# Kernel tuning notes

Hardware: AMD Instinct MI355X
Metric: run time of the kernel (lower is better)

Reference implementation:

```python
import jax, jax.numpy as jnp
import numpy as np

D = 1024
S = 4096

def setup_inputs() -> dict:
    key = jax.random.key(0)
    ks = jax.random.split(key, 7)
    x = jax.random.normal(ks[0], (S, D), dtype=jnp.float32)
    scale = 1.0 / np.sqrt(D)
    wq = jax.random.normal(ks[1], (D, D), dtype=jnp.float32) * scale
    wk = jax.random.normal(ks[2], (D, D), dtype=jnp.float32) * scale
    wv = jax.random.normal(ks[3], (D, D), dtype=jnp.float32) * scale
    bq = jax.random.normal(ks[4], (D,), dtype=jnp.float32) * 0.01
    bk = jax.random.normal(ks[5], (D,), dtype=jnp.float32) * 0.01
    bv = jax.random.normal(ks[6], (D,), dtype=jnp.float32) * 0.01
    return {"x": x, "wq": wq, "bq": bq, "wk": wk, "bk": bk, "wv": wv, "bv": bv}

def reference(x, wq, bq, wk, bk, wv, bv):
    # q = x @ wq^T + bq  (torch nn.Linear convention: weight [out,in])
    q = x @ wq.T + bq            # [S, D]
    k = x @ wk.T + bk            # [S, D]
    v = x @ wv.T + bv            # [S, D]
    inv_sqrt_d = 1.0 / jnp.sqrt(jnp.asarray(x.shape[1], dtype=x.dtype))
    scores = (q @ k.T) * inv_sqrt_d      # [S, S]
    attn = jax.nn.softmax(scores, axis=-1)
    return attn @ v                      # [S, D]
```

## Files before the change

### kernel.cpp

```cpp
#include <hip/hip_runtime.h>
#include <stdint.h>
#include <stddef.h>

#define SEQ 4096
#define DIM 1024

typedef __bf16 bf16x8 __attribute__((ext_vector_type(8)));
typedef float floatx4 __attribute__((ext_vector_type(4)));
typedef unsigned short u16x8 __attribute__((ext_vector_type(8)));

__device__ __forceinline__ unsigned short f2b(float f) {
  union { float f; unsigned u; } v; v.f = f;
  unsigned u = v.u;
  unsigned r = (u + 0x7FFFu + ((u >> 16) & 1u)) >> 16;
  return (unsigned short)r;
}
__device__ __forceinline__ float b2f(unsigned short h) {
  union { unsigned u; float f; } v; v.u = ((unsigned)h) << 16;
  return v.f;
}

__global__ __launch_bounds__(256)
void cvt_all(const float* __restrict__ x, const float* __restrict__ wq,
             const float* __restrict__ wk, const float* __restrict__ wv,
             unsigned short* __restrict__ xb, unsigned short* __restrict__ wqb,
             unsigned short* __restrict__ wkb, unsigned short* __restrict__ wvb) {
  const int bid = blockIdx.x;
  const float* src;
  unsigned short* dst;
  int off;
  if (bid < 4096)      { src = x;  dst = xb;  off = bid; }
  else if (bid < 5120) { src = wq; dst = wqb; off = bid - 4096; }
  else if (bid < 6144) { src = wk; dst = wkb; off = bid - 5120; }
  else                 { src = wv; dst = wvb; off = bid - 6144; }
  const int i = off * 1024 + threadIdx.x * 4;
  float4 f = *(const float4*)(src + i);
  ushort4 o;
  o.x = f2b(f.x); o.y = f2b(f.y); o.z = f2b(f.z); o.w = f2b(f.w);
  *(ushort4*)(dst + i) = o;
}

__device__ __forceinline__ void swizzle_tiles(int gx, int gy, int& bx, int& by) {
  const int pid = blockIdx.y * gx + blockIdx.x;
  const int GM = 8;
  const int group = pid / (GM * gx);
  const int first = group * GM;
  const int gsz = (gy - first) < GM ? (gy - first) : GM;
  by = first + (pid % gsz);
  bx = (pid % (GM * gx)) / gsz;
}

__device__ __forceinline__ void gemm_core128(
    const unsigned short* __restrict__ A,
    const unsigned short* __restrict__ B,
    int lda, int ldb, int kext,
    unsigned short* As, unsigned short* Bs,
    floatx4 acc[4][4]) {
  const int tid  = threadIdx.x;
  const int lane = tid & 63;
  const int wave = tid >> 6;
  const int sub_m = (wave >> 1) * 64;
  const int sub_n = (wave & 1) * 64;
  const int col  = lane & 15;
  const int quad = lane >> 4;

  const int srow  = tid >> 3;
  const int sgran = (tid & 7) ^ (srow & 7);
  const int scol  = sgran * 8;
  const int dflat = tid * 8;

  const unsigned short* Ag = A + (size_t)srow * lda + scol;
  const unsigned short* Bg = B + (size_t)srow * ldb + scol;

  for (int k0 = 0; k0 < kext; k0 += 64) {
    __syncthreads();
#pragma unroll
    for (int j = 0; j < 4; j++) {
      __builtin_amdgcn_global_load_lds(
          (const __attribute__((address_space(1))) void*)(Ag + (size_t)(j * 32) * lda + k0),
          (__attribute__((address_space(3))) void*)(&As[j * 2048 + dflat]), 16, 0, 0);
      __builtin_amdgcn_global_load_lds(
          (const __attribute__((address_space(1))) void*)(Bg + (size_t)(j * 32) * ldb + k0),
          (__attribute__((address_space(3))) void*)(&Bs[j * 2048 + dflat]), 16, 0, 0);
    }
    __syncthreads();
#pragma unroll
    for (int ks = 0; ks < 64; ks += 32) {
      const int gbase = ks >> 3;
      bf16x8 af[4], bfr[4];
#pragma unroll
      for (int i = 0; i < 4; i++) {
        const int R = sub_m + 16 * i + col;
        const int slot = (gbase + quad) ^ (R & 7);
        af[i] = *(const bf16x8*)&As[R * 64 + slot * 8];
      }
#pragma unroll
      for (int j = 0; j < 4; j++) {
        const int R = sub_n + 16 * j + col;
        const int slot = (gbase + quad) ^ (R & 7);
        bfr[j] = *(const bf16x8*)&Bs[R * 64 + slot * 8];
      }
#pragma unroll
      for (int i = 0; i < 4; i++)
#pragma unroll
        for (int j = 0; j < 4; j++)
          acc[i][j] = __builtin_amdgcn_mfma_f32_16x16x32_bf16(af[i], bfr[j],
                                                              acc[i][j], 0, 0, 0);
    }
  }
}

__device__ __forceinline__ void gemm_core64(
    const unsigned short* __restrict__ A,
    const unsigned short* __restrict__ B,
    int lda, int ldb, int kext,
    unsigned short* As, unsigned short* Bs,
    floatx4 acc[4][2]) {
  const int tid  = threadIdx.x;
  const int lane = tid & 63;
  const int wave = tid >> 6;
  const int sub_n = wave * 32;
  const int col  = lane & 15;
  const int quad = lane >> 4;

  const int srow  = tid >> 3;
  const int sgran = (tid & 7) ^ (srow & 7);
  const int scol  = sgran * 8;
  const int dflat = tid * 8;

  const unsigned short* Ag = A + (size_t)srow * lda + scol;
  const unsigned short* Bg = B + (size_t)srow * ldb + scol;

  for (int k0 = 0; k0 < kext; k0 += 64) {
    __syncthreads();
#pragma unroll
    for (int j = 0; j < 2; j++)
      __builtin_amdgcn_global_load_lds(
          (const __attribute__((address_space(1))) void*)(Ag + (size_t)(j * 32) * lda + k0),
          (__attribute__((address_space(3))) void*)(&As[j * 2048 + dflat]), 16, 0, 0);
#pragma unroll
    for (int j = 0; j < 4; j++)
      __builtin_amdgcn_global_load_lds(
          (const __attribute__((address_space(1))) void*)(Bg + (size_t)(j * 32) * ldb + k0),
          (__attribute__((address_space(3))) void*)(&Bs[j * 2048 + dflat]), 16, 0, 0);
    __syncthreads();
#pragma unroll
    for (int ks = 0; ks < 64; ks += 32) {
      const int gbase = ks >> 3;
      bf16x8 af[4], bfr[2];
#pragma unroll
      for (int i = 0; i < 4; i++) {
        const int R = 16 * i + col;
        const int slot = (gbase + quad) ^ (R & 7);
        af[i] = *(const bf16x8*)&As[R * 64 + slot * 8];
      }
#pragma unroll
      for (int j = 0; j < 2; j++) {
        const int R = sub_n + 16 * j + col;
        const int slot = (gbase + quad) ^ (R & 7);
        bfr[j] = *(const bf16x8*)&Bs[R * 64 + slot * 8];
      }
#pragma unroll
      for (int i = 0; i < 4; i++)
#pragma unroll
        for (int j = 0; j < 2; j++)
          acc[i][j] = __builtin_amdgcn_mfma_f32_16x16x32_bf16(af[i], bfr[j],
                                                              acc[i][j], 0, 0, 0);
    }
  }
}


__global__ __launch_bounds__(256, 2)
void qkv_gemm(const unsigned short* __restrict__ xb,
              const unsigned short* __restrict__ wqb,
              const unsigned short* __restrict__ wkb,
              const unsigned short* __restrict__ wvb,
              const float* __restrict__ bq, const float* __restrict__ bk,
              const float* __restrict__ bv,
              unsigned short* __restrict__ qb, unsigned short* __restrict__ kb,
              unsigned short* __restrict__ vtb) {
  __shared__ unsigned short As[8192];
  __shared__ unsigned short Bs[8192];
  const int z = blockIdx.z;
  const int pid = blockIdx.x;

  floatx4 acc[4][4];
#pragma unroll
  for (int i = 0; i < 4; i++)
#pragma unroll
    for (int j = 0; j < 4; j++) acc[i][j] = (floatx4)0.0f;

  const int lane = threadIdx.x & 63;
  const int wave = threadIdx.x >> 6;
  const int sub_m = (wave >> 1) * 64;
  const int sub_n = (wave & 1) * 64;
  const int col  = lane & 15;
  const int quad = lane >> 4;

  if (z < 2) {
    const unsigned short* W = z ? wkb : wqb;
    const float* bias = z ? bk : bq;
    unsigned short* outp = z ? kb : qb;
    const int by = pid >> 3, bx = pid & 7;
    const int tile_m = by * 128, tile_n = bx * 128;

    gemm_core128(xb + (size_t)tile_m * DIM, W + (size_t)tile_n * DIM,
                 DIM, DIM, DIM, As, Bs, acc);

    float biasv[4];
#pragma unroll
    for (int j = 0; j < 4; j++) biasv[j] = bias[tile_n + sub_n + 16 * j + col];
#pragma unroll
    for (int i = 0; i < 4; i++)
#pragma unroll
      for (int j = 0; j < 4; j++)
#pragma unroll
        for (int r = 0; r < 4; r++) {
          const int m = tile_m + sub_m + 16 * i + quad * 4 + r;
          const int n = tile_n + sub_n + 16 * j + col;
          outp[(size_t)m * DIM + n] = f2b(acc[i][j][r] + biasv[j]);
        }
  } else {
    const int by = pid >> 5, bx = pid & 31;
    const int tile_m = by * 128, tile_n = bx * 128;

    gemm_core128(wvb + (size_t)tile_m * DIM, xb + (size_t)tile_n * DIM,
                 DIM, DIM, DIM, As, Bs, acc);

#pragma unroll
    for (int i = 0; i < 4; i++) {
      const float* bp = &bv[tile_m + sub_m + 16 * i + quad * 4];
      float bm[4];
#pragma unroll
      for (int r = 0; r < 4; r++) bm[r] = bp[r];
#pragma unroll
      for (int j = 0; j < 4; j++)
#pragma unroll
        for (int r = 0; r < 4; r++) {
          const int m = tile_m + sub_m + 16 * i + quad * 4 + r;
          const int n = tile_n + sub_n + 16 * j + col;
          vtb[(size_t)m * SEQ + n] = f2b(acc[i][j][r] + bm[r]);
        }
    }
  }
}

__global__ __launch_bounds__(256, 2)
void score_gemm(const unsigned short* __restrict__ qb,
                const unsigned short* __restrict__ kb,
                unsigned short* __restrict__ sc, float scale) {
  __shared__ unsigned short As[8192];
  __shared__ unsigned short Bs[8192];
  int bx, by;
  swizzle_tiles(gridDim.x, gridDim.y, bx, by);
  const int tile_m = by * 128;
  const int tile_n = bx * 128;

  floatx4 acc[4][4];
#pragma unroll
  for (int i = 0; i < 4; i++)
#pragma unroll
    for (int j = 0; j < 4; j++) acc[i][j] = (floatx4)0.0f;

  gemm_core128(qb + (size_t)tile_m * DIM, kb + (size_t)tile_n * DIM,
               DIM, DIM, DIM, As, Bs, acc);

  const int lane = threadIdx.x & 63;
  const int wave = threadIdx.x >> 6;
  const int sub_m = (wave >> 1) * 64;
  const int sub_n = (wave & 1) * 64;
  const int col  = lane & 15;
  const int quad = lane >> 4;
#pragma unroll
  for (int i = 0; i < 4; i++)
#pragma unroll
    for (int j = 0; j < 4; j++)
#pragma unroll
      for (int r = 0; r < 4; r++) {
        const int m = tile_m + sub_m + 16 * i + quad * 4 + r;
        const int n = tile_n + sub_n + 16 * j + col;
        sc[(size_t)m * SEQ + n] = f2b(acc[i][j][r] * scale);
      }
}

__global__ __launch_bounds__(256, 2)
void pv_gemm(const unsigned short* __restrict__ sc,
             const unsigned short* __restrict__ vtb,
             float* __restrict__ out) {
  __shared__ unsigned short As[4096];
  __shared__ unsigned short Bs[8192];
  const int tile_m = blockIdx.y * 64;
  const int tile_n = blockIdx.x * 128;

  floatx4 acc[4][2];
#pragma unroll
  for (int i = 0; i < 4; i++)
#pragma unroll
    for (int j = 0; j < 2; j++) acc[i][j] = (floatx4)0.0f;

  gemm_core64(sc + (size_t)tile_m * SEQ, vtb + (size_t)tile_n * SEQ,
              SEQ, SEQ, SEQ, As, Bs, acc);

  const int lane = threadIdx.x & 63;
  const int wave = threadIdx.x >> 6;
  const int sub_n = wave * 32;
  const int col  = lane & 15;
  const int quad = lane >> 4;
#pragma unroll
  for (int i = 0; i < 4; i++)
#pragma unroll
    for (int j = 0; j < 2; j++)
#pragma unroll
      for (int r = 0; r < 4; r++) {
        const int m = tile_m + 16 * i + quad * 4 + r;
        const int n = tile_n + sub_n + 16 * j + col;
        out[(size_t)m * DIM + n] = acc[i][j][r];
      }
}

__global__ __launch_bounds__(256)
void softmax_inplace(unsigned short* __restrict__ P) {
  const int row = blockIdx.x;
  unsigned short* p = P + (size_t)row * SEQ;
  const int tid  = threadIdx.x;
  const int lane = tid & 63;
  const int wave = tid >> 6;

  u16x8 raw0 = *(const u16x8*)(p + tid * 16);
  u16x8 raw1 = *(const u16x8*)(p + tid * 16 + 8);
  float v[16];
#pragma unroll
  for (int k = 0; k < 8; k++) v[k] = b2f(raw0[k]);
#pragma unroll
  for (int k = 0; k < 8; k++) v[8 + k] = b2f(raw1[k]);

  float mx = -1e30f;
#pragma unroll
  for (int k = 0; k < 16; k++) mx = fmaxf(mx, v[k]);
#pragma unroll
  for (int off = 32; off > 0; off >>= 1) mx = fmaxf(mx, __shfl_xor(mx, off, 64));
  __shared__ float redm[4];
  __shared__ float reds[4];
  if (lane == 0) redm[wave] = mx;
  __syncthreads();
  mx = fmaxf(fmaxf(redm[0], redm[1]), fmaxf(redm[2], redm[3]));

  float sum = 0.0f;
#pragma unroll
  for (int k = 0; k < 16; k++) {
    v[k] = exp2f((v[k] - mx) * 1.44269504f);
    sum += v[k];
  }
#pragma unroll
  for (int off = 32; off > 0; off >>= 1) sum += __shfl_xor(sum, off, 64);
  if (lane == 0) reds[wave] = sum;
  __syncthreads();
  sum = reds[0] + reds[1] + reds[2] + reds[3];
  const float inv = 1.0f / sum;

  u16x8 o0, o1;
#pragma unroll
  for (int k = 0; k < 8; k++) o0[k] = f2b(v[k] * inv);
#pragma unroll
  for (int k = 0; k < 8; k++) o1[k] = f2b(v[8 + k] * inv);
  *(u16x8*)(p + tid * 16) = o0;
  *(u16x8*)(p + tid * 16 + 8) = o1;
}

extern "C" void kernel_launch(void* const* d_in, const int* in_sizes, int n_in,
                              void* d_out, int out_size, void* d_ws, size_t ws_size,
                              hipStream_t stream) {
  const float* x  = (const float*)d_in[0];
  const float* wq = (const float*)d_in[1];
  const float* bq = (const float*)d_in[2];
  const float* wk = (const float*)d_in[3];
  const float* bk = (const float*)d_in[4];
  const float* wv = (const float*)d_in[5];
  const float* bv = (const float*)d_in[6];

  uint8_t* ws = (uint8_t*)d_ws;
  unsigned short* xb  = (unsigned short*)(ws);
  unsigned short* wqb = (unsigned short*)(ws + ((size_t)8  << 20));
  unsigned short* wkb = (unsigned short*)(ws + ((size_t)10 << 20));
  unsigned short* wvb = (unsigned short*)(ws + ((size_t)12 << 20));
  unsigned short* qb  = (unsigned short*)(ws + ((size_t)14 << 20));
  unsigned short* kb  = (unsigned short*)(ws + ((size_t)22 << 20));
  unsigned short* vtb = (unsigned short*)(ws + ((size_t)30 << 20));
  unsigned short* sc  = (unsigned short*)(ws + ((size_t)38 << 20));

  cvt_all<<<7168, 256, 0, stream>>>(x, wq, wk, wv, xb, wqb, wkb, wvb);

  qkv_gemm<<<dim3(256, 1, 3), 256, 0, stream>>>(
      xb, wqb, wkb, wvb, bq, bk, bv, qb, kb, vtb);

  score_gemm<<<dim3(SEQ / 128, SEQ / 128), 256, 0, stream>>>(qb, kb, sc, 0.03125f);

  softmax_inplace<<<SEQ, 256, 0, stream>>>(sc);

  pv_gemm<<<dim3(DIM / 128, SEQ / 64), 256, 0, stream>>>(sc, vtb, (float*)d_out);
}
```

Baseline: 223.8 us.

## Use split-K 128x128 tiles for PV GEMM and XCD-aware score tile mapping

The PV GEMM moves from 64x128 tiles to 128x128 tiles, which doubles operand reuse. To keep the grid large it splits K into two halves across blockIdx.z, writing partial sums to the output and to a workspace buffer that a new reduce_add kernel then sums. The score GEMM's tile swizzle is replaced by an explicit mapping that groups column tiles per XCD to improve L2 locality. In exchange this adds an extra kernel launch plus a 16MB read/write pass for the reduction. The partial buffer reuses the xb workspace region, which is no longer needed at that point.

```diff
diff --git a/kernel.cpp b/kernel.cpp
--- a/kernel.cpp
+++ b/kernel.cpp
@@ -110,66 +110,6 @@
   }
 }
 
-__device__ __forceinline__ void gemm_core64(
-    const unsigned short* __restrict__ A,
-    const unsigned short* __restrict__ B,
-    int lda, int ldb, int kext,
-    unsigned short* As, unsigned short* Bs,
-    floatx4 acc[4][2]) {
-  const int tid  = threadIdx.x;
-  const int lane = tid & 63;
-  const int wave = tid >> 6;
-  const int sub_n = wave * 32;
-  const int col  = lane & 15;
-  const int quad = lane >> 4;
-
-  const int srow  = tid >> 3;
-  const int sgran = (tid & 7) ^ (srow & 7);
-  const int scol  = sgran * 8;
-  const int dflat = tid * 8;
-
-  const unsigned short* Ag = A + (size_t)srow * lda + scol;
-  const unsigned short* Bg = B + (size_t)srow * ldb + scol;
-
-  for (int k0 = 0; k0 < kext; k0 += 64) {
-    __syncthreads();
-#pragma unroll
-    for (int j = 0; j < 2; j++)
-      __builtin_amdgcn_global_load_lds(
-          (const __attribute__((address_space(1))) void*)(Ag + (size_t)(j * 32) * lda + k0),
-          (__attribute__((address_space(3))) void*)(&As[j * 2048 + dflat]), 16, 0, 0);
-#pragma unroll
-    for (int j = 0; j < 4; j++)
-      __builtin_amdgcn_global_load_lds(
-          (const __attribute__((address_space(1))) void*)(Bg + (size_t)(j * 32) * ldb + k0),
-          (__attribute__((address_space(3))) void*)(&Bs[j * 2048 + dflat]), 16, 0, 0);
-    __syncthreads();
-#pragma unroll
-    for (int ks = 0; ks < 64; ks += 32) {
-      const int gbase = ks >> 3;
-      bf16x8 af[4], bfr[2];
-#pragma unroll
-      for (int i = 0; i < 4; i++) {
-        const int R = 16 * i + col;
-        const int slot = (gbase + quad) ^ (R & 7);
-        af[i] = *(const bf16x8*)&As[R * 64 + slot * 8];
-      }
-#pragma unroll
-      for (int j = 0; j < 2; j++) {
-        const int R = sub_n + 16 * j + col;
-        const int slot = (gbase + quad) ^ (R & 7);
-        bfr[j] = *(const bf16x8*)&Bs[R * 64 + slot * 8];
-      }
-#pragma unroll
-      for (int i = 0; i < 4; i++)
-#pragma unroll
-        for (int j = 0; j < 2; j++)
-          acc[i][j] = __builtin_amdgcn_mfma_f32_16x16x32_bf16(af[i], bfr[j],
-                                                              acc[i][j], 0, 0, 0);
-    }
-  }
-}
-
 
 __global__ __launch_bounds__(256, 2)
 void qkv_gemm(const unsigned short* __restrict__ xb,
@@ -252,8 +192,11 @@
                 unsigned short* __restrict__ sc, float scale) {
   __shared__ unsigned short As[8192];
   __shared__ unsigned short Bs[8192];
-  int bx, by;
-  swizzle_tiles(gridDim.x, gridDim.y, bx, by);
+  const int pid = blockIdx.y * gridDim.x + blockIdx.x;
+  const int xcd = pid & 7;
+  const int local = pid >> 3;
+  const int bx = xcd * 4 + (local & 3);
+  const int by = local >> 2;
   const int tile_m = by * 128;
   const int tile_n = bx * 128;
 
@@ -287,36 +230,52 @@
 __global__ __launch_bounds__(256, 2)
 void pv_gemm(const unsigned short* __restrict__ sc,
              const unsigned short* __restrict__ vtb,
-             float* __restrict__ out) {
-  __shared__ unsigned short As[4096];
+             float* __restrict__ out0, float* __restrict__ out1) {
+  __shared__ unsigned short As[8192];
   __shared__ unsigned short Bs[8192];
-  const int tile_m = blockIdx.y * 64;
-  const int tile_n = blockIdx.x * 128;
-
-  floatx4 acc[4][2];
-#pragma unroll
-  for (int i = 0; i < 4; i++)
-#pragma unroll
-    for (int j = 0; j < 2; j++) acc[i][j] = (floatx4)0.0f;
-
-  gemm_core64(sc + (size_t)tile_m * SEQ, vtb + (size_t)tile_n * SEQ,
-              SEQ, SEQ, SEQ, As, Bs, acc);
+  const int z = blockIdx.z;
+  const int koff = z * (SEQ / 2);
+  float* C = z ? out1 : out0;
+  int bx, by;
+  swizzle_tiles(gridDim.x, gridDim.y, bx, by);
+  const int tile_m = by * 128;
+  const int tile_n = bx * 128;
+
+  floatx4 acc[4][4];
+#pragma unroll
+  for (int i = 0; i < 4; i++)
+#pragma unroll
+    for (int j = 0; j < 4; j++) acc[i][j] = (floatx4)0.0f;
+
+  gemm_core128(sc + (size_t)tile_m * SEQ + koff,
+               vtb + (size_t)tile_n * SEQ + koff,
+               SEQ, SEQ, SEQ / 2, As, Bs, acc);
 
   const int lane = threadIdx.x & 63;
   const int wave = threadIdx.x >> 6;
-  const int sub_n = wave * 32;
+  const int sub_m = (wave >> 1) * 64;
+  const int sub_n = (wave & 1) * 64;
   const int col  = lane & 15;
   const int quad = lane >> 4;
 #pragma unroll
   for (int i = 0; i < 4; i++)
 #pragma unroll
-    for (int j = 0; j < 2; j++)
+    for (int j = 0; j < 4; j++)
 #pragma unroll
       for (int r = 0; r < 4; r++) {
-        const int m = tile_m + 16 * i + quad * 4 + r;
+        const int m = tile_m + sub_m + 16 * i + quad * 4 + r;
         const int n = tile_n + sub_n + 16 * j + col;
-        out[(size_t)m * DIM + n] = acc[i][j][r];
+        C[(size_t)m * DIM + n] = acc[i][j][r];
       }
+}
+
+__global__ __launch_bounds__(256)
+void reduce_add(float* __restrict__ out, const float* __restrict__ part) {
+  const int i = (blockIdx.x * 256 + threadIdx.x) * 4;
+  float4 a = *(const float4*)(out + i);
+  float4 b = *(const float4*)(part + i);
+  a.x += b.x; a.y += b.y; a.z += b.z; a.w += b.w;
+  *(float4*)(out + i) = a;
 }
 
 __global__ __launch_bounds__(256)
@@ -388,6 +347,7 @@
   unsigned short* kb  = (unsigned short*)(ws + ((size_t)22 << 20));
   unsigned short* vtb = (unsigned short*)(ws + ((size_t)30 << 20));
   unsigned short* sc  = (unsigned short*)(ws + ((size_t)38 << 20));
+  float*          part = (float*)(ws);
 
   cvt_all<<<7168, 256, 0, stream>>>(x, wq, wk, wv, xb, wqb, wkb, wvb);
 
@@ -398,5 +358,8 @@
 
   softmax_inplace<<<SEQ, 256, 0, stream>>>(sc);
 
-  pv_gemm<<<dim3(DIM / 128, SEQ / 64), 256, 0, stream>>>(sc, vtb, (float*)d_out);
-}
+  pv_gemm<<<dim3(DIM / 128, SEQ / 128, 2), 256, 0, stream>>>(
+      sc, vtb, (float*)d_out, part);
+
+  reduce_add<<<(SEQ * DIM) / 1024, 256, 0, stream>>>((float*)d_out, part);
+}
```

After: 205.6 us. -8.2%, faster.
